# Optimization experiments

Measured on AMD Instinct MI355X. Metric: run time of the kernel, lower is better.

## Reference

```python
import jax, jax.numpy as jnp
import numpy as np

N = 100000   # nodes
E = 800000   # edges
D = 128      # input dim
H = 128      # hidden dim
C = 2        # output classes
BN_EPS = 1e-5


def setup_inputs() -> dict:
    key = jax.random.key(0)
    ks = jax.random.split(key, 24)
    glorot = lambda k, shape: jax.random.normal(k, shape, dtype=jnp.float32) * np.sqrt(2.0 / (shape[0] + shape[1]))
    inp = {
        "x": jax.random.normal(ks[0], (N, D), dtype=jnp.float32),
        "edge_index": jax.random.randint(ks[1], (2, E), 0, N, dtype=jnp.int64),
        "W0": glorot(ks[2], (D, H)), "b0": jnp.zeros((H,), jnp.float32),
        "W1": glorot(ks[3], (H, H)), "b1": jnp.zeros((H,), jnp.float32),
        "W2": glorot(ks[4], (H, H)), "b2": jnp.zeros((H,), jnp.float32),
        "W3": glorot(ks[5], (H, C)), "b3": jnp.zeros((C,), jnp.float32),
        # BatchNorm (eval mode: running stats)
        "bn0_g": jax.random.normal(ks[6], (H,), dtype=jnp.float32) * 0.1 + 1.0,
        "bn0_b": jax.random.normal(ks[7], (H,), dtype=jnp.float32) * 0.1,
        "bn0_m": jax.random.normal(ks[8], (H,), dtype=jnp.float32) * 0.1,
        "bn0_v": jax.random.uniform(ks[9], (H,), dtype=jnp.float32) + 0.5,
        "bn1_g": jax.random.normal(ks[10], (H,), dtype=jnp.float32) * 0.1 + 1.0,
        "bn1_b": jax.random.normal(ks[11], (H,), dtype=jnp.float32) * 0.1,
        "bn1_m": jax.random.normal(ks[12], (H,), dtype=jnp.float32) * 0.1,
        "bn1_v": jax.random.uniform(ks[13], (H,), dtype=jnp.float32) + 0.5,
    }
    return inp


def _gcn_conv(h, W, b, src, dst, norm, self_norm):
    # GCNConv: D^-1/2 (A + I) D^-1/2 (h W) + b
    hw = h @ W                                             # [N, out]
    msg = hw[src] * norm[:, None]                          # [E, out] gather
    agg = jax.ops.segment_sum(msg, dst, num_segments=N)    # [N, out] scatter-add
    return agg + hw * self_norm[:, None] + b


def _bn_eval(h, g, b, m, v):
    return (h - m) * (g * jax.lax.rsqrt(v + BN_EPS)) + b


def reference(x, edge_index, W0, b0, W1, b1, W2, b2, W3, b3,
              bn0_g, bn0_b, bn0_m, bn0_v, bn1_g, bn1_b, bn1_m, bn1_v):
    src, dst = edge_index[0], edge_index[1]
    # symmetric normalization with self-loops
    deg = jax.ops.segment_sum(jnp.ones((E,), jnp.float32), dst, num_segments=N) + 1.0
    dis = jax.lax.rsqrt(deg)                 # deg >= 1, no inf
    norm = dis[src] * dis[dst]               # per-edge norm
    self_norm = dis * dis                    # self-loop norm

    # layer 0 (eval mode: dropout is identity)
    h = jax.nn.relu(_gcn_conv(x, W0, b0, src, dst, norm, self_norm))
    # layer 1: conv -> bn -> relu -> residual
    h_prev = h
    h = _gcn_conv(h, W1, b1, src, dst, norm, self_norm)
    h = jax.nn.relu(_bn_eval(h, bn0_g, bn0_b, bn0_m, bn0_v)) + h_prev
    # layer 2
    h_prev = h
    h = _gcn_conv(h, W2, b2, src, dst, norm, self_norm)
    h = jax.nn.relu(_bn_eval(h, bn1_g, bn1_b, bn1_m, bn1_v)) + h_prev
    # output layer
    h = _gcn_conv(h, W3, b3, src, dst, norm, self_norm)
    return jax.nn.log_softmax(h, axis=1)
```

## Files before the change

kernel.cpp:

```cpp
#include <hip/hip_runtime.h>
#include <hip/hip_bf16.h>
#include <type_traits>

#define NN 100000
#define NE 800000
#define HD 128
#define BN_EPS 1e-5f

typedef __bf16 bf16x8 __attribute__((ext_vector_type(8)));
typedef float  f32x4  __attribute__((ext_vector_type(4)));
typedef float  f32x2  __attribute__((ext_vector_type(2)));


__global__ __launch_bounds__(256) void count_k(const int* __restrict__ ei, int* __restrict__ count,
                                               int* __restrict__ rank) {
    int e = blockIdx.x * 256 + threadIdx.x;
    if (e < NE) rank[e] = atomicAdd(&count[ei[NE + e]], 1);
}

__global__ __launch_bounds__(256) void bnpre_k(const float* __restrict__ g0, const float* __restrict__ b0,
                                               const float* __restrict__ m0, const float* __restrict__ v0,
                                               const float* __restrict__ g1, const float* __restrict__ b1,
                                               const float* __restrict__ m1, const float* __restrict__ v1,
                                               float* __restrict__ A0, float* __restrict__ B0,
                                               float* __restrict__ A1, float* __restrict__ B1) {
    int t = threadIdx.x;
    if (t < 128) {
        float a = g0[t] * rsqrtf(v0[t] + BN_EPS);
        A0[t] = a; B0[t] = b0[t] - m0[t] * a;
    } else {
        int u = t - 128;
        float a = g1[u] * rsqrtf(v1[u] + BN_EPS);
        A1[u] = a; B1[u] = b1[u] - m1[u] * a;
    }
}

__global__ __launch_bounds__(256) void prepw_k(const float* __restrict__ W0, const float* __restrict__ W1,
                                               const float* __restrict__ W2, __bf16* __restrict__ WT) {
    const float* Ws[3] = {W0, W1, W2};
    const float* W = Ws[blockIdx.x];
    __bf16* T = WT + blockIdx.x * (HD * HD);
    int tid = threadIdx.x;
    #pragma unroll
    for (int it = 0; it < 64; ++it) {
        int idx = it * 256 + tid;
        int n = idx >> 7, k = idx & 127;
        T[idx] = (__bf16)W[k * HD + n];
    }
}

__global__ __launch_bounds__(256) void scan1_k(const int* __restrict__ count,
                                               int* __restrict__ rp, int* __restrict__ bsums,
                                               float* __restrict__ dis, float* __restrict__ selfn) {
    __shared__ int sm[256];
    int tid = threadIdx.x;
    int i = blockIdx.x * 256 + tid;
    int v = (i < NN) ? count[i] : 0;
    if (i < NN) {
        float deg = (float)v + 1.0f;
        float di = rsqrtf(deg);
        dis[i] = di;
        selfn[i] = di * di;
    }
    sm[tid] = v; __syncthreads();
    for (int off = 1; off < 256; off <<= 1) {
        int t = (tid >= off) ? sm[tid - off] : 0;
        __syncthreads();
        sm[tid] += t;
        __syncthreads();
    }
    if (i < NN) rp[i] = sm[tid] - v;
    if (tid == 255) bsums[blockIdx.x] = sm[tid];
}

__global__ __launch_bounds__(512) void scan2_k(int* __restrict__ bsums, int nb) {
    __shared__ int sm[512];
    int tid = threadIdx.x;
    int v = (tid < nb) ? bsums[tid] : 0;
    sm[tid] = v; __syncthreads();
    for (int off = 1; off < 512; off <<= 1) {
        int t = (tid >= off) ? sm[tid - off] : 0;
        __syncthreads();
        sm[tid] += t;
        __syncthreads();
    }
    if (tid < nb) bsums[tid] = sm[tid] - v;
}

__global__ __launch_bounds__(256) void scan3_k(int* __restrict__ rp, const int* __restrict__ bsums) {
    int i = blockIdx.x * 256 + threadIdx.x;
    if (i < NN) rp[i] += bsums[blockIdx.x];
    if (i == 0) rp[NN] = NE;
}

__global__ __launch_bounds__(256) void scatter_k(const int* __restrict__ ei, const int* __restrict__ rp,
                                                 const int* __restrict__ rank, const float* __restrict__ dis,
                                                 uint2* __restrict__ edges) {
    int e = blockIdx.x * 256 + threadIdx.x;
    if (e >= NE) return;
    int s = ei[e], d = ei[NE + e];
    int pos = rp[d] + rank[e];
    edges[pos] = make_uint2((unsigned)s, __float_as_uint(dis[s] * dis[d]));
}


#define WROW 136

template <typename T>
__global__ __launch_bounds__(256, 4) void gemm128_k(const T* __restrict__ A, const __bf16* __restrict__ WTg,
                                                    __bf16* __restrict__ HW) {
    __shared__ __bf16 WL[128 * WROW];
    const int tid = threadIdx.x;
    const int wid  = __builtin_amdgcn_readfirstlane(tid >> 6);
    const int lane = tid & 63;
    const int m = lane & 15, quad = lane >> 4;
    const int row_base = blockIdx.x * 64 + wid * 16;

    int r = row_base + m;
    if (r >= NN) r = NN - 1;
    bf16x8 afr[4];
    if constexpr (std::is_same<T, float>::value) {
        const float4* ap = (const float4*)(A + (size_t)r * HD);
        #pragma unroll
        for (int ks = 0; ks < 4; ++ks) {
            float4 x0 = ap[ks * 8 + quad * 2], x1 = ap[ks * 8 + quad * 2 + 1];
            bf16x8 a;
            a[0] = (__bf16)x0.x; a[1] = (__bf16)x0.y; a[2] = (__bf16)x0.z; a[3] = (__bf16)x0.w;
            a[4] = (__bf16)x1.x; a[5] = (__bf16)x1.y; a[6] = (__bf16)x1.z; a[7] = (__bf16)x1.w;
            afr[ks] = a;
        }
    } else {
        const bf16x8* ap = (const bf16x8*)(A + (size_t)r * HD);
        #pragma unroll
        for (int ks = 0; ks < 4; ++ks) afr[ks] = ap[ks * 4 + quad];
    }

    #pragma unroll
    for (int it = 0; it < 8; ++it) {
        int id = it * 256 + tid;
        int n = id >> 4, c = id & 15;
        *(uint4*)&WL[n * WROW + c * 8] = *(const uint4*)(WTg + n * HD + c * 8);
    }
    __syncthreads();

    f32x4 acc[8];
    #pragma unroll
    for (int ct = 0; ct < 8; ++ct) acc[ct] = (f32x4){0.f, 0.f, 0.f, 0.f};

    #pragma unroll
    for (int ks = 0; ks < 4; ++ks) {
        const int k0 = ks * 32 + quad * 8;
        #pragma unroll
        for (int ct = 0; ct < 8; ++ct) {
            bf16x8 bfr = *(const bf16x8*)&WL[(ct * 16 + m) * WROW + k0];
            acc[ct] = __builtin_amdgcn_mfma_f32_16x16x32_bf16(afr[ks], bfr, acc[ct], 0, 0, 0);
        }
    }

    #pragma unroll
    for (int ct = 0; ct < 8; ++ct)
        #pragma unroll
        for (int rr = 0; rr < 4; ++rr) {
            int row = row_base + quad * 4 + rr;
            if (row < NN) HW[(size_t)row * HD + ct * 16 + m] = (__bf16)acc[ct][rr];
        }
}


__device__ __forceinline__ void acc8p(f32x2* acc, uint4 rv, float wt) {
    f32x2 w2 = {wt, wt};
    f32x2 x0 = {__uint_as_float(rv.x << 16), __uint_as_float(rv.x & 0xffff0000u)};
    f32x2 x1 = {__uint_as_float(rv.y << 16), __uint_as_float(rv.y & 0xffff0000u)};
    f32x2 x2 = {__uint_as_float(rv.z << 16), __uint_as_float(rv.z & 0xffff0000u)};
    f32x2 x3 = {__uint_as_float(rv.w << 16), __uint_as_float(rv.w & 0xffff0000u)};
    acc[0] = __builtin_elementwise_fma(x0, w2, acc[0]);
    acc[1] = __builtin_elementwise_fma(x1, w2, acc[1]);
    acc[2] = __builtin_elementwise_fma(x2, w2, acc[2]);
    acc[3] = __builtin_elementwise_fma(x3, w2, acc[3]);
}

__device__ __forceinline__ void unpack8(uint4 rv, float* f) {
    f[0] = __uint_as_float(rv.x << 16);         f[1] = __uint_as_float(rv.x & 0xffff0000u);
    f[2] = __uint_as_float(rv.y << 16);         f[3] = __uint_as_float(rv.y & 0xffff0000u);
    f[4] = __uint_as_float(rv.z << 16);         f[5] = __uint_as_float(rv.z & 0xffff0000u);
    f[6] = __uint_as_float(rv.w << 16);         f[7] = __uint_as_float(rv.w & 0xffff0000u);
}

template <int MODE>
__global__ __launch_bounds__(256) void agg_k(const __bf16* __restrict__ hw, const int* __restrict__ rp,
                                             const uint2* __restrict__ edges,
                                             const float* __restrict__ selfn, const float* __restrict__ bias,
                                             const float* __restrict__ bnA, const float* __restrict__ bnB,
                                             __bf16* __restrict__ hb, const float* __restrict__ W3,
                                             float2* __restrict__ hw3) {
    const int lane = threadIdx.x & 63;
    const int wid  = threadIdx.x >> 6;
    const int grp  = lane >> 4;
    const int m    = lane & 15;
    const int n = blockIdx.x * 16 + wid * 4 + grp;
    const int c0 = m * 8;
    const int L = NE - 1;

    const int e0 = rp[n], e1 = rp[n + 1];

    const float sn = selfn[n];
    uint4 rv_self = *(const uint4*)(hw + ((size_t)n << 7) + c0);
    __bf16* hbp = hb + ((size_t)n << 7) + c0;
    uint4 rv_prev;
    if (MODE != 0) rv_prev = *(const uint4*)hbp;

    f32x2 acc2[4];
    #pragma unroll
    for (int j = 0; j < 4; ++j) acc2[j] = (f32x2){0.f, 0.f};

    int e = e0;
    int cnt = e1 - e0;
    uint2 edA = edges[min(e,     L)];
    uint2 edB = edges[min(e + 1, L)];
    uint2 edC = edges[min(e + 2, L)];
    uint2 edD = edges[min(e + 3, L)];
    while (cnt >= 4) {
        uint4 r0 = *(const uint4*)(hw + ((size_t)edA.x << 7) + c0);
        uint4 r1 = *(const uint4*)(hw + ((size_t)edB.x << 7) + c0);
        uint4 r2 = *(const uint4*)(hw + ((size_t)edC.x << 7) + c0);
        uint4 r3 = *(const uint4*)(hw + ((size_t)edD.x << 7) + c0);
        uint2 nA = edges[min(e + 4, L)];
        uint2 nB = edges[min(e + 5, L)];
        uint2 nC = edges[min(e + 6, L)];
        uint2 nD = edges[min(e + 7, L)];
        acc8p(acc2, r0, __uint_as_float(edA.y));
        acc8p(acc2, r1, __uint_as_float(edB.y));
        acc8p(acc2, r2, __uint_as_float(edC.y));
        acc8p(acc2, r3, __uint_as_float(edD.y));
        edA = nA; edB = nB; edC = nC; edD = nD;
        e += 4; cnt -= 4;
    }
    if (cnt >= 2) {
        uint4 r0 = *(const uint4*)(hw + ((size_t)edA.x << 7) + c0);
        uint4 r1 = *(const uint4*)(hw + ((size_t)edB.x << 7) + c0);
        acc8p(acc2, r0, __uint_as_float(edA.y));
        acc8p(acc2, r1, __uint_as_float(edB.y));
        edA = edC;
        cnt -= 2;
    }
    if (cnt == 1) {
        uint4 rv = *(const uint4*)(hw + ((size_t)edA.x << 7) + c0);
        acc8p(acc2, rv, __uint_as_float(edA.y));
    }
    acc8p(acc2, rv_self, sn);

    float acc[8] = {acc2[0][0], acc2[0][1], acc2[1][0], acc2[1][1],
                    acc2[2][0], acc2[2][1], acc2[3][0], acc2[3][1]};

    float4 bs0 = *(const float4*)(bias + c0);
    float4 bs1 = *(const float4*)(bias + c0 + 4);
    float z[8] = {acc[0] + bs0.x, acc[1] + bs0.y, acc[2] + bs0.z, acc[3] + bs0.w,
                  acc[4] + bs1.x, acc[5] + bs1.y, acc[6] + bs1.z, acc[7] + bs1.w};

    if (MODE == 0) {
        bf16x8 v;
        #pragma unroll
        for (int j = 0; j < 8; ++j) v[j] = (__bf16)fmaxf(z[j], 0.f);
        *(bf16x8*)hbp = v;
    } else {
        float4 a0v = *(const float4*)(bnA + c0), a1v = *(const float4*)(bnA + c0 + 4);
        float4 b0v = *(const float4*)(bnB + c0), b1v = *(const float4*)(bnB + c0 + 4);
        float Af[8] = {a0v.x, a0v.y, a0v.z, a0v.w, a1v.x, a1v.y, a1v.z, a1v.w};
        float Bf[8] = {b0v.x, b0v.y, b0v.z, b0v.w, b1v.x, b1v.y, b1v.z, b1v.w};
        float pr[8];
        unpack8(rv_prev, pr);
        float hn[8];
        #pragma unroll
        for (int j = 0; j < 8; ++j)
            hn[j] = fmaxf(fmaf(z[j], Af[j], Bf[j]), 0.f) + pr[j];

        if (MODE == 1) {
            bf16x8 v;
            #pragma unroll
            for (int j = 0; j < 8; ++j) v[j] = (__bf16)hn[j];
            *(bf16x8*)hbp = v;
        } else {
            float4 w0 = *(const float4*)(W3 + c0 * 2);
            float4 w1 = *(const float4*)(W3 + c0 * 2 + 4);
            float4 w2 = *(const float4*)(W3 + c0 * 2 + 8);
            float4 w3v = *(const float4*)(W3 + c0 * 2 + 12);
            float p0 = hn[0] * w0.x + hn[1] * w0.z + hn[2] * w1.x + hn[3] * w1.z
                     + hn[4] * w2.x + hn[5] * w2.z + hn[6] * w3v.x + hn[7] * w3v.z;
            float p1 = hn[0] * w0.y + hn[1] * w0.w + hn[2] * w1.y + hn[3] * w1.w
                     + hn[4] * w2.y + hn[5] * w2.w + hn[6] * w3v.y + hn[7] * w3v.w;
            #pragma unroll
            for (int o = 1; o < 16; o <<= 1) {
                p0 += __shfl_xor(p0, o);
                p1 += __shfl_xor(p1, o);
            }
            if (m == 0) hw3[n] = make_float2(p0, p1);
        }
    }
}


__global__ __launch_bounds__(256) void final_k(const float2* __restrict__ hw3, const int* __restrict__ rp,
                                               const uint2* __restrict__ edges,
                                               const float* __restrict__ selfn, const float* __restrict__ b3,
                                               float* __restrict__ out) {
    int n = blockIdx.x * 256 + threadIdx.x;
    if (n >= NN) return;
    float a0 = 0.f, a1 = 0.f;
    int e1 = rp[n + 1];
    for (int e = rp[n]; e < e1; ++e) {
        uint2 ed = edges[e];
        float w = __uint_as_float(ed.y);
        float2 v = hw3[ed.x];
        a0 = fmaf(w, v.x, a0);
        a1 = fmaf(w, v.y, a1);
    }
    float sn = selfn[n];
    float2 hv = hw3[n];
    float z0 = a0 + sn * hv.x + b3[0];
    float z1 = a1 + sn * hv.y + b3[1];
    float mx = fmaxf(z0, z1);
    float l = mx + logf(expf(z0 - mx) + expf(z1 - mx));
    out[n * 2 + 0] = z0 - l;
    out[n * 2 + 1] = z1 - l;
}


extern "C" void kernel_launch(void* const* d_in, const int* in_sizes, int n_in,
                              void* d_out, int out_size, void* d_ws, size_t ws_size,
                              hipStream_t stream) {
    (void)in_sizes; (void)n_in; (void)out_size; (void)ws_size;

    const float* x   = (const float*)d_in[0];
    const int*   ei  = (const int*)d_in[1];
    const float* W0  = (const float*)d_in[2];
    const float* b0  = (const float*)d_in[3];
    const float* W1  = (const float*)d_in[4];
    const float* b1  = (const float*)d_in[5];
    const float* W2  = (const float*)d_in[6];
    const float* b2  = (const float*)d_in[7];
    const float* W3  = (const float*)d_in[8];
    const float* b3  = (const float*)d_in[9];
    const float* bn0g = (const float*)d_in[10];
    const float* bn0b = (const float*)d_in[11];
    const float* bn0m = (const float*)d_in[12];
    const float* bn0v = (const float*)d_in[13];
    const float* bn1g = (const float*)d_in[14];
    const float* bn1b = (const float*)d_in[15];
    const float* bn1m = (const float*)d_in[16];
    const float* bn1v = (const float*)d_in[17];
    float* out = (float*)d_out;

    char* p = (char*)d_ws;
    auto alloc = [&](size_t bytes) -> void* {
        void* r = (void*)p;
        p += (bytes + 255) & ~(size_t)255;
        return r;
    };
    __bf16*  hb    = (__bf16*)alloc((size_t)NN * HD * 2);
    __bf16*  hw    = (__bf16*)alloc((size_t)NN * HD * 2);
    float2*  hw3   = (float2*)alloc((size_t)NN * 8);
    float*   dis   = (float*)alloc((size_t)NN * 4);
    float*   selfn = (float*)alloc((size_t)NN * 4);
    int*     count = (int*)alloc((size_t)NN * 4);
    int*     rp    = (int*)alloc((size_t)(NN + 1) * 4);
    uint2*   edges = (uint2*)alloc((size_t)NE * 8);
    int*     rank  = (int*)alloc((size_t)NE * 4);
    int*     bsums = (int*)alloc((size_t)512 * 4);
    float*   bnA0  = (float*)alloc(128 * 4);
    float*   bnB0  = (float*)alloc(128 * 4);
    float*   bnA1  = (float*)alloc(128 * 4);
    float*   bnB1  = (float*)alloc(128 * 4);
    __bf16*  WT    = (__bf16*)alloc((size_t)3 * HD * HD * 2);

    const int NB_E = (NE + 255) / 256;
    const int NB_N = (NN + 255) / 256;
    const int NB_G = (NN + 63) / 64;
    const int NB_A = (NN + 15) / 16;

    hipMemsetAsync(count, 0, (size_t)NN * 4, stream);

    count_k<<<NB_E, 256, 0, stream>>>(ei, count, rank);
    prepw_k<<<3, 256, 0, stream>>>(W0, W1, W2, WT);
    bnpre_k<<<1, 256, 0, stream>>>(bn0g, bn0b, bn0m, bn0v, bn1g, bn1b, bn1m, bn1v,
                                   bnA0, bnB0, bnA1, bnB1);
    scan1_k<<<NB_N, 256, 0, stream>>>(count, rp, bsums, dis, selfn);
    scan2_k<<<1, 512, 0, stream>>>(bsums, NB_N);
    scan3_k<<<NB_N, 256, 0, stream>>>(rp, bsums);
    scatter_k<<<NB_E, 256, 0, stream>>>(ei, rp, rank, dis, edges);

    gemm128_k<float><<<NB_G, 256, 0, stream>>>(x, WT, hw);
    agg_k<0><<<NB_A, 256, 0, stream>>>(hw, rp, edges, selfn, b0,
                                       nullptr, nullptr, hb, nullptr, nullptr);
    gemm128_k<__bf16><<<NB_G, 256, 0, stream>>>(hb, WT + HD * HD, hw);
    agg_k<1><<<NB_A, 256, 0, stream>>>(hw, rp, edges, selfn, b1,
                                       bnA0, bnB0, hb, nullptr, nullptr);
    gemm128_k<__bf16><<<NB_G, 256, 0, stream>>>(hb, WT + 2 * HD * HD, hw);
    agg_k<2><<<NB_A, 256, 0, stream>>>(hw, rp, edges, selfn, b2,
                                       bnA1, bnB1, hb, W3, hw3);
    final_k<<<NB_N, 256, 0, stream>>>(hw3, rp, edges, selfn, b3, out);
}
```

Measured before the change: 345.9 us.

## Sort nodes by in-degree for balanced aggregation and merge scan passes

Builds a permutation of nodes bucketed by in-degree using a histogram, a 64-bin scan and a scatter. The aggregation and final kernels then process nodes in that order, so lanes in a wavefront walk edge lists of similar length and less work is lost to divergence. The second and third prefix-scan kernels are merged into one that has each block reduce the preceding block sums itself. This adds three small preprocessing kernels and an indirection through perm, and it scatters the writes to hb/hw3 rows, costing some memory locality.

```diff
diff --git a/kernel.cpp b/kernel.cpp
--- a/kernel.cpp
+++ b/kernel.cpp
@@ -73,23 +73,21 @@
     if (tid == 255) bsums[blockIdx.x] = sm[tid];
 }
 
-__global__ __launch_bounds__(512) void scan2_k(int* __restrict__ bsums, int nb) {
-    __shared__ int sm[512];
+__global__ __launch_bounds__(256) void scan23_k(int* __restrict__ rp, const int* __restrict__ bsums, int nb) {
+    __shared__ int sm[256];
     int tid = threadIdx.x;
-    int v = (tid < nb) ? bsums[tid] : 0;
-    sm[tid] = v; __syncthreads();
-    for (int off = 1; off < 512; off <<= 1) {
-        int t = (tid >= off) ? sm[tid - off] : 0;
+    int b = blockIdx.x;
+    int partial = 0;
+    for (int i = tid; i < b; i += 256) partial += bsums[i];
+    sm[tid] = partial; __syncthreads();
+    #pragma unroll
+    for (int off = 128; off > 0; off >>= 1) {
+        if (tid < off) sm[tid] += sm[tid + off];
         __syncthreads();
-        sm[tid] += t;
-        __syncthreads();
-    }
-    if (tid < nb) bsums[tid] = sm[tid] - v;
-}
-
-__global__ __launch_bounds__(256) void scan3_k(int* __restrict__ rp, const int* __restrict__ bsums) {
-    int i = blockIdx.x * 256 + threadIdx.x;
-    if (i < NN) rp[i] += bsums[blockIdx.x];
+    }
+    int prefix = sm[0];
+    int i = b * 256 + tid;
+    if (i < NN) rp[i] += prefix;
     if (i == 0) rp[NN] = NE;
 }
 
@@ -101,6 +99,46 @@
     int s = ei[e], d = ei[NE + e];
     int pos = rp[d] + rank[e];
     edges[pos] = make_uint2((unsigned)s, __float_as_uint(dis[s] * dis[d]));
+}
+
+
+__global__ __launch_bounds__(256) void dhist_k(const int* __restrict__ count, int* __restrict__ rank2,
+                                               int* __restrict__ gcnt) {
+    __shared__ int lh[64];
+    __shared__ int lbase[64];
+    int tid = threadIdx.x;
+    if (tid < 64) lh[tid] = 0;
+    __syncthreads();
+    int i = blockIdx.x * 256 + tid;
+    int bin = 0, myrank = 0;
+    if (i < NN) {
+        bin = min(count[i], 63);
+        myrank = atomicAdd(&lh[bin], 1);
+    }
+    __syncthreads();
+    if (tid < 64) lbase[tid] = lh[tid] ? atomicAdd(&gcnt[tid], lh[tid]) : 0;
+    __syncthreads();
+    if (i < NN) rank2[i] = lbase[bin] + myrank;
+}
+
+__global__ __launch_bounds__(64) void dscan_k(const int* __restrict__ gcnt, int* __restrict__ binoff) {
+    int t = threadIdx.x;
+    int v = gcnt[t];
+    int x = v;
+    #pragma unroll
+    for (int off = 1; off < 64; off <<= 1) {
+        int y = __shfl_up(x, off);
+        if (t >= off) x += y;
+    }
+    binoff[t] = x - v;
+}
+
+__global__ __launch_bounds__(256) void dperm_k(const int* __restrict__ count, const int* __restrict__ rank2,
+                                               const int* __restrict__ binoff, int* __restrict__ perm) {
+    int i = blockIdx.x * 256 + threadIdx.x;
+    if (i >= NN) return;
+    int bin = min(count[i], 63);
+    perm[binoff[bin] + rank2[i]] = i;
 }
 
 
@@ -188,7 +226,7 @@
 
 template <int MODE>
 __global__ __launch_bounds__(256) void agg_k(const __bf16* __restrict__ hw, const int* __restrict__ rp,
-                                             const uint2* __restrict__ edges,
+                                             const uint2* __restrict__ edges, const int* __restrict__ perm,
                                              const float* __restrict__ selfn, const float* __restrict__ bias,
                                              const float* __restrict__ bnA, const float* __restrict__ bnB,
                                              __bf16* __restrict__ hb, const float* __restrict__ W3,
@@ -197,7 +235,7 @@
     const int wid  = threadIdx.x >> 6;
     const int grp  = lane >> 4;
     const int m    = lane & 15;
-    const int n = blockIdx.x * 16 + wid * 4 + grp;
+    const int n = perm[blockIdx.x * 16 + wid * 4 + grp];
     const int c0 = m * 8;
     const int L = NE - 1;
 
@@ -300,11 +338,12 @@
 
 
 __global__ __launch_bounds__(256) void final_k(const float2* __restrict__ hw3, const int* __restrict__ rp,
-                                               const uint2* __restrict__ edges,
+                                               const uint2* __restrict__ edges, const int* __restrict__ perm,
                                                const float* __restrict__ selfn, const float* __restrict__ b3,
                                                float* __restrict__ out) {
-    int n = blockIdx.x * 256 + threadIdx.x;
-    if (n >= NN) return;
+    int i = blockIdx.x * 256 + threadIdx.x;
+    if (i >= NN) return;
+    int n = perm[i];
     float a0 = 0.f, a1 = 0.f;
     int e1 = rp[n + 1];
     for (int e = rp[n]; e < e1; ++e) {
@@ -362,9 +401,13 @@
     float*   dis   = (float*)alloc((size_t)NN * 4);
     float*   selfn = (float*)alloc((size_t)NN * 4);
     int*     count = (int*)alloc((size_t)NN * 4);
+    int*     gcnt  = (int*)alloc((size_t)64 * 4);
     int*     rp    = (int*)alloc((size_t)(NN + 1) * 4);
     uint2*   edges = (uint2*)alloc((size_t)NE * 8);
     int*     rank  = (int*)alloc((size_t)NE * 4);
+    int*     rank2 = (int*)alloc((size_t)NN * 4);
+    int*     perm  = (int*)alloc((size_t)NN * 4);
+    int*     binoff= (int*)alloc((size_t)64 * 4);
     int*     bsums = (int*)alloc((size_t)512 * 4);
     float*   bnA0  = (float*)alloc(128 * 4);
     float*   bnB0  = (float*)alloc(128 * 4);
@@ -377,25 +420,27 @@
     const int NB_G = (NN + 63) / 64;
     const int NB_A = (NN + 15) / 16;
 
-    hipMemsetAsync(count, 0, (size_t)NN * 4, stream);
+    hipMemsetAsync(count, 0, (size_t)NN * 4 + 256, stream);
 
     count_k<<<NB_E, 256, 0, stream>>>(ei, count, rank);
     prepw_k<<<3, 256, 0, stream>>>(W0, W1, W2, WT);
     bnpre_k<<<1, 256, 0, stream>>>(bn0g, bn0b, bn0m, bn0v, bn1g, bn1b, bn1m, bn1v,
                                    bnA0, bnB0, bnA1, bnB1);
     scan1_k<<<NB_N, 256, 0, stream>>>(count, rp, bsums, dis, selfn);
-    scan2_k<<<1, 512, 0, stream>>>(bsums, NB_N);
-    scan3_k<<<NB_N, 256, 0, stream>>>(rp, bsums);
+    scan23_k<<<NB_N, 256, 0, stream>>>(rp, bsums, NB_N);
     scatter_k<<<NB_E, 256, 0, stream>>>(ei, rp, rank, dis, edges);
+    dhist_k<<<NB_N, 256, 0, stream>>>(count, rank2, gcnt);
+    dscan_k<<<1, 64, 0, stream>>>(gcnt, binoff);
+    dperm_k<<<NB_N, 256, 0, stream>>>(count, rank2, binoff, perm);
 
     gemm128_k<float><<<NB_G, 256, 0, stream>>>(x, WT, hw);
-    agg_k<0><<<NB_A, 256, 0, stream>>>(hw, rp, edges, selfn, b0,
+    agg_k<0><<<NB_A, 256, 0, stream>>>(hw, rp, edges, perm, selfn, b0,
                                        nullptr, nullptr, hb, nullptr, nullptr);
     gemm128_k<__bf16><<<NB_G, 256, 0, stream>>>(hb, WT + HD * HD, hw);
-    agg_k<1><<<NB_A, 256, 0, stream>>>(hw, rp, edges, selfn, b1,
+    agg_k<1><<<NB_A, 256, 0, stream>>>(hw, rp, edges, perm, selfn, b1,
                                        bnA0, bnB0, hb, nullptr, nullptr);
     gemm128_k<__bf16><<<NB_G, 256, 0, stream>>>(hb, WT + 2 * HD * HD, hw);
-    agg_k<2><<<NB_A, 256, 0, stream>>>(hw, rp, edges, selfn, b2,
+    agg_k<2><<<NB_A, 256, 0, stream>>>(hw, rp, edges, perm, selfn, b2,
                                        bnA1, bnB1, hb, W3, hw3);
-    final_k<<<NB_N, 256, 0, stream>>>(hw3, rp, edges, selfn, b3, out);
-}
+    final_k<<<NB_N, 256, 0, stream>>>(hw3, rp, edges, perm, selfn, b3, out);
+}
```

Measured after the change: 361.5 us. 4.5% more time.
